# Performance work log

Hardware: AMD Instinct MI355X
Metric: run time of the kernel (lower is better)

## Reference

```python
import jax, jax.numpy as jnp
import numpy as np

B, N, DIM = 4, 2048, 512
HEADS, DIM_HEAD = 8, 64
INNER = HEADS * DIM_HEAD  # == DIM, so to_out is Identity
LN_EPS = 1e-5
MASK_FILL = 1e-8  # faithful to torch.where(mask, attn, 1e-08)


def setup_inputs() -> dict:
    key = jax.random.key(0)
    k1, k2 = jax.random.split(key)
    x = jax.random.normal(k1, (B, N, DIM), dtype=jnp.float32)
    gamma = jnp.ones((DIM,), dtype=jnp.float32)
    beta = jnp.zeros((DIM,), dtype=jnp.float32)
    w_qkv = jax.random.normal(k2, (3 * INNER, DIM), dtype=jnp.float32) * (DIM ** -0.5)
    mask = jnp.tril(jnp.ones((N, N), dtype=bool))  # causal boolean mask, asserted 2-D in source
    return {"x": x, "gamma": gamma, "beta": beta, "w_qkv": w_qkv, "mask": mask}


def reference(x, gamma, beta, w_qkv, mask):
    # LayerNorm over last dim
    mu = jnp.mean(x, axis=-1, keepdims=True)
    var = jnp.var(x, axis=-1, keepdims=True)
    h = (x - mu) * jax.lax.rsqrt(var + LN_EPS) * gamma + beta
    # qkv projection (no bias), chunk into q, k, v
    qkv = h @ w_qkv.T  # [B, N, 3*INNER]
    q, k, v = jnp.split(qkv, 3, axis=-1)

    def to_heads(t):  # b n (h d) -> b h n d
        return t.reshape(B, N, HEADS, DIM_HEAD).transpose(0, 2, 1, 3)

    q, k, v = to_heads(q), to_heads(k), to_heads(v)
    # NOTE: original forward does NOT apply self.scale
    attn = jnp.einsum('bhnd,bhmd->bhnm', q, k)
    attn = jnp.where(mask[None, None, :, :], attn, MASK_FILL)
    p = jax.nn.softmax(attn, axis=-1)
    out = jnp.einsum('bhnm,bhmd->bhnd', p, v)
    out = out.transpose(0, 2, 1, 3).reshape(B, N, INNER)  # b h n d -> b n (h d)
    return out  # to_out is Identity since INNER == DIM
```

## Files before the change

### kernel.cpp

```cpp
#include <hip/hip_runtime.h>
#include <hip/hip_bf16.h>
#include <math.h>

#define B_  4
#define N_  2048
#define DIM_ 512
#define HEADS_ 8
#define QKV_ 1536
#define MASK_C 1e-8f
#define M_FIX 12.0f
#define LOG2E 1.44269504f

typedef __bf16 bf16_t;
typedef bf16_t bf16x8 __attribute__((ext_vector_type(8)));
typedef float  f32x4  __attribute__((ext_vector_type(4)));

__device__ __forceinline__ bf16_t f2b(float x) { return (bf16_t)x; }
__device__ __forceinline__ float  b2f(bf16_t x) { return (float)x; }

__device__ __forceinline__ f32x4 mfma16(bf16x8 a, bf16x8 b, f32x4 c) {
    return __builtin_amdgcn_mfma_f32_16x16x32_bf16(a, b, c, 0, 0, 0);
}

__global__ __launch_bounds__(256) void ln_wsplit_kernel(const float* __restrict__ x,
                                                        const float* __restrict__ gamma,
                                                        const float* __restrict__ beta,
                                                        bf16_t* __restrict__ hh,
                                                        bf16_t* __restrict__ hl,
                                                        const float* __restrict__ wq,
                                                        bf16_t* __restrict__ wh,
                                                        bf16_t* __restrict__ wl) {
    int blk = blockIdx.x;
    int t = threadIdx.x;
    if (blk >= B_ * N_) {
        int i = ((blk - B_ * N_) * 256 + t) * 4;
        float4 v = *(const float4*)&wq[i];
        float vv[4] = {v.x, v.y, v.z, v.w};
        #pragma unroll
        for (int j = 0; j < 4; j++) {
            bf16_t hi = f2b(vv[j]);
            wh[i + j] = hi;
            wl[i + j] = f2b(vv[j] - b2f(hi));
        }
        return;
    }
    int row = blk;
    const float* xr = x + (size_t)row * DIM_;
    float2 xv = *(const float2*)&xr[2 * t];
    float e0 = xv.x, e1 = xv.y;
    float s  = e0 + e1;
    float sq = e0 * e0 + e1 * e1;
    for (int off = 32; off; off >>= 1) {
        s  += __shfl_xor(s, off);
        sq += __shfl_xor(sq, off);
    }
    __shared__ float red[8];
    int w = t >> 6;
    if ((t & 63) == 0) { red[w] = s; red[4 + w] = sq; }
    __syncthreads();
    float S  = red[0] + red[1] + red[2] + red[3];
    float SQ = red[4] + red[5] + red[6] + red[7];
    float mu = S * (1.0f / DIM_);
    float var = SQ * (1.0f / DIM_) - mu * mu;
    float rs = rsqrtf(var + 1e-5f);
    float2 gv = *(const float2*)&gamma[2 * t];
    float2 bv = *(const float2*)&beta[2 * t];
    float y0 = (e0 - mu) * rs * gv.x + bv.x;
    float y1 = (e1 - mu) * rs * gv.y + bv.y;
    size_t base = (size_t)row * DIM_ + 2 * t;
    bf16_t h0 = f2b(y0), h1 = f2b(y1);
    __align__(4) bf16_t hp[2] = {h0, h1};
    __align__(4) bf16_t lp[2] = {f2b(y0 - b2f(h0)), f2b(y1 - b2f(h1))};
    *(unsigned int*)&hh[base] = *(unsigned int*)hp;
    *(unsigned int*)&hl[base] = *(unsigned int*)lp;
}

__global__ __launch_bounds__(256, 3) void qkv_gemm(const bf16_t* __restrict__ hh,
                                                   const bf16_t* __restrict__ hl,
                                                   const bf16_t* __restrict__ wh,
                                                   const bf16_t* __restrict__ wl,
                                                   bf16_t* __restrict__ qh, bf16_t* __restrict__ ql,
                                                   bf16_t* __restrict__ kh, bf16_t* __restrict__ kl,
                                                   bf16_t* __restrict__ vth,
                                                   float* __restrict__ part) {
    __shared__ __align__(16) bf16_t smem[20480];
    bf16_t* Ah = smem;
    bf16_t* Al = smem + 5120;
    bf16_t* Bh = smem + 10240;
    bf16_t* Bl = smem + 15360;
    int bm = blockIdx.x & 63;
    int bn = blockIdx.x >> 6;
    int t = threadIdx.x;
    int w = t >> 6, lane = t & 63, quad = lane >> 4, l16 = lane & 15;

    f32x4 acc[2][8];
    #pragma unroll
    for (int i = 0; i < 2; i++)
        #pragma unroll
        for (int j = 0; j < 8; j++) acc[i][j] = (f32x4)(0.0f);

    int sr = t >> 1, skc = (t & 1) * 16;
    size_t gA = (size_t)(bm * 128 + sr) * 512 + skc;
    size_t gB = (size_t)(bn * 128 + sr) * 512 + skc;

    uint4 rAh0 = *(const uint4*)&hh[gA];
    uint4 rAh1 = *(const uint4*)&hh[gA + 8];
    uint4 rAl0 = *(const uint4*)&hl[gA];
    uint4 rAl1 = *(const uint4*)&hl[gA + 8];
    uint4 rBh0 = *(const uint4*)&wh[gB];
    uint4 rBh1 = *(const uint4*)&wh[gB + 8];
    uint4 rBl0 = *(const uint4*)&wl[gB];
    uint4 rBl1 = *(const uint4*)&wl[gB + 8];

    for (int k0 = 0; k0 < 512; k0 += 32) {
        __syncthreads();
        *(uint4*)&Ah[sr * 40 + skc]     = rAh0;
        *(uint4*)&Ah[sr * 40 + skc + 8] = rAh1;
        *(uint4*)&Al[sr * 40 + skc]     = rAl0;
        *(uint4*)&Al[sr * 40 + skc + 8] = rAl1;
        *(uint4*)&Bh[sr * 40 + skc]     = rBh0;
        *(uint4*)&Bh[sr * 40 + skc + 8] = rBh1;
        *(uint4*)&Bl[sr * 40 + skc]     = rBl0;
        *(uint4*)&Bl[sr * 40 + skc + 8] = rBl1;
        __syncthreads();

        if (k0 < 480) {
            int kn = k0 + 32;
            rAh0 = *(const uint4*)&hh[gA + kn];
            rAh1 = *(const uint4*)&hh[gA + kn + 8];
            rAl0 = *(const uint4*)&hl[gA + kn];
            rAl1 = *(const uint4*)&hl[gA + kn + 8];
            rBh0 = *(const uint4*)&wh[gB + kn];
            rBh1 = *(const uint4*)&wh[gB + kn + 8];
            rBl0 = *(const uint4*)&wl[gB + kn];
            rBl1 = *(const uint4*)&wl[gB + kn + 8];
        }

        bf16x8 aH[2], aL[2];
        #pragma unroll
        for (int mt = 0; mt < 2; mt++) {
            aH[mt] = *(const bf16x8*)&Ah[(w * 32 + mt * 16 + l16) * 40 + quad * 8];
            aL[mt] = *(const bf16x8*)&Al[(w * 32 + mt * 16 + l16) * 40 + quad * 8];
        }
        #pragma unroll
        for (int nt = 0; nt < 8; nt++) {
            bf16x8 bH = *(const bf16x8*)&Bh[(nt * 16 + l16) * 40 + quad * 8];
            bf16x8 bL = *(const bf16x8*)&Bl[(nt * 16 + l16) * 40 + quad * 8];
            #pragma unroll
            for (int mt = 0; mt < 2; mt++) {
                acc[mt][nt] = mfma16(aH[mt], bH, acc[mt][nt]);
                acc[mt][nt] = mfma16(aH[mt], bL, acc[mt][nt]);
                acc[mt][nt] = mfma16(aL[mt], bH, acc[mt][nt]);
            }
        }
    }

    if (bn < 8) {
        #pragma unroll
        for (int mt = 0; mt < 2; mt++)
            #pragma unroll
            for (int nt = 0; nt < 8; nt++)
                #pragma unroll
                for (int reg = 0; reg < 4; reg++) {
                    float v = acc[mt][nt][reg];
                    int row = bm * 128 + w * 32 + mt * 16 + quad * 4 + reg;
                    int n = bn * 128 + nt * 16 + l16;
                    bf16_t hi = f2b(v);
                    bf16_t lo = f2b(v - b2f(hi));
                    if (n < 512) {
                        size_t a = (size_t)row * 512 + n;
                        qh[a] = hi; ql[a] = lo;
                    } else {
                        size_t a = (size_t)row * 512 + (n - 512);
                        kh[a] = hi; kl[a] = lo;
                    }
                }
    } else {
        int bb = bm >> 4, key0 = (bm & 15) * 128;
        int n = t & 127, mc = (t >> 7) * 64;
        int head = (bn - 8) * 2 + (n >> 6), dd = n & 63;
        size_t obase = ((size_t)((bb * 8 + head) * 64 + dd)) * 2048 + key0 + mc;
        float Ssum = 0.0f;
        #pragma unroll
        for (int pass = 0; pass < 2; pass++) {
            __syncthreads();
            #pragma unroll
            for (int mt = 0; mt < 2; mt++)
                #pragma unroll
                for (int nt = 0; nt < 8; nt++)
                    #pragma unroll
                    for (int reg = 0; reg < 4; reg++) {
                        float v = acc[mt][nt][reg];
                        bf16_t hi = f2b(v);
                        bf16_t val = pass ? f2b(v - b2f(hi)) : hi;
                        smem[(w * 32 + mt * 16 + quad * 4 + reg) * 132 + nt * 16 + l16] = val;
                    }
            __syncthreads();
            #pragma unroll
            for (int i = 0; i < 64; i += 8) {
                __align__(16) bf16_t v8[8];
                #pragma unroll
                for (int j = 0; j < 8; j++) {
                    v8[j] = smem[(mc + i + j) * 132 + n];
                    Ssum += b2f(v8[j]);
                }
                if (pass == 0)
                    *(uint4*)&vth[obase + i] = *(const uint4*)v8;
            }
        }
        int tt = (key0 >> 6) + (mc >> 6);
        part[((size_t)((bb * 8 + head) * 32 + tt)) * 64 + dd] = Ssum;
    }
}

__global__ __launch_bounds__(256, 4) void attn_kernel(const bf16_t* __restrict__ qh,
                                                      const bf16_t* __restrict__ ql,
                                                      const bf16_t* __restrict__ kh,
                                                      const bf16_t* __restrict__ kl,
                                                      const bf16_t* __restrict__ vth,
                                                      const float* __restrict__ part,
                                                      float* __restrict__ out) {
    __shared__ __align__(16) bf16_t smem[17152];
    __shared__ float sufl[4][64];
    char* lds = (char*)smem;
    bf16_t* Ps = smem + 12288;

    int blk = blockIdx.x;
    int bh = blk & 31;
    int gi = blk >> 5;
    int g3 = gi & 7;
    int q4 = gi >> 3;
    int rt;
    if (q4 == 0)      rt = 31 - g3;
    else if (q4 == 1) rt = g3;
    else if (q4 == 2) rt = 23 - g3;
    else              rt = 8 + g3;
    int b = bh >> 3, head = bh & 7;
    int t = threadIdx.x;
    int w = t >> 6, lane = t & 63, quad = lane >> 4, l16 = lane & 15;

    {
        int d = t & 63, g = t >> 6;
        float s = 0.0f;
        for (int tt = rt + 1 + g; tt < 32; tt += 4)
            s += part[((size_t)bh * 32 + tt) * 64 + d];
        sufl[g][d] = s;
    }

    bf16x8 qAH[2], qAL[2];
    {
        int qrow = rt * 64 + w * 16 + l16;
        size_t g = ((size_t)(b * N_ + qrow)) * 512 + head * 64 + quad * 8;
        qAH[0] = *(const bf16x8*)&qh[g];
        qAH[1] = *(const bf16x8*)&qh[g + 32];
        qAL[0] = *(const bf16x8*)&ql[g];
        qAL[1] = *(const bf16x8*)&ql[g + 32];
    }
    bf16x8 ones;
    #pragma unroll
    for (int j = 0; j < 8; j++) ones[j] = f2b(1.0f);

    f32x4 O[4];
    #pragma unroll
    for (int nt = 0; nt < 4; nt++) O[nt] = (f32x4)(0.0f);
    f32x4 Lacc = (f32x4)(0.0f);
    const float mbias = M_FIX * LOG2E;

    int r = t >> 2, c16 = t & 3;
    int swz = (r & 7) << 4;
    int lk0 = r * 128 + ((c16 * 32)      ^ swz);
    int lk1 = r * 128 + ((c16 * 32 + 16) ^ swz);
    size_t gk = ((size_t)(b * N_ + r)) * 512 + head * 64 + c16 * 16;
    size_t gv = ((size_t)(bh * 64 + r)) * 2048 + c16 * 16;

    uint4 pKh0 = *(const uint4*)&kh[gk];
    uint4 pKh1 = *(const uint4*)&kh[gk + 8];
    uint4 pKl0 = *(const uint4*)&kl[gk];
    uint4 pKl1 = *(const uint4*)&kl[gk + 8];
    uint4 pVh0 = *(const uint4*)&vth[gv];
    uint4 pVh1 = *(const uint4*)&vth[gv + 8];

    for (int jt = 0; jt <= rt; jt++) {
        __syncthreads();
        *(uint4*)(lds + lk0)         = pKh0;
        *(uint4*)(lds + lk1)         = pKh1;
        *(uint4*)(lds + 8192 + lk0)  = pKl0;
        *(uint4*)(lds + 8192 + lk1)  = pKl1;
        *(uint4*)(lds + 16384 + lk0) = pVh0;
        *(uint4*)(lds + 16384 + lk1) = pVh1;
        __syncthreads();

        if (jt < rt) {
            gk += (size_t)64 * 512;
            gv += 64;
            pKh0 = *(const uint4*)&kh[gk];
            pKh1 = *(const uint4*)&kh[gk + 8];
            pKl0 = *(const uint4*)&kl[gk];
            pKl1 = *(const uint4*)&kl[gk + 8];
            pVh0 = *(const uint4*)&vth[gv];
            pVh1 = *(const uint4*)&vth[gv + 8];
        }

        f32x4 S[4];
        #pragma unroll
        for (int nt = 0; nt < 4; nt++) S[nt] = (f32x4)(0.0f);
        __builtin_amdgcn_s_setprio(1);
        #pragma unroll
        for (int khf = 0; khf < 2; khf++) {
            #pragma unroll
            for (int nt = 0; nt < 4; nt++) {
                int row = nt * 16 + l16;
                int bc = (khf * 64 + quad * 16) ^ ((row & 7) << 4);
                bf16x8 bH = *(const bf16x8*)(lds + row * 128 + bc);
                bf16x8 bL = *(const bf16x8*)(lds + 8192 + row * 128 + bc);
                S[nt] = mfma16(qAH[khf], bH, S[nt]);
                S[nt] = mfma16(qAH[khf], bL, S[nt]);
                S[nt] = mfma16(qAL[khf], bH, S[nt]);
            }
        }
        __builtin_amdgcn_s_setprio(0);

        if (jt == rt) {
            int lrow = w * 16 + quad * 4;
            #pragma unroll
            for (int nt = 0; nt < 4; nt++)
                #pragma unroll
                for (int reg = 0; reg < 4; reg++)
                    if (nt * 16 + l16 > lrow + reg) S[nt][reg] = MASK_C;
        }

        #pragma unroll
        for (int nt = 0; nt < 4; nt++)
            #pragma unroll
            for (int reg = 0; reg < 4; reg++)
                Ps[(w * 16 + quad * 4 + reg) * 76 + nt * 16 + l16] =
                    f2b(exp2f(fmaf(S[nt][reg], LOG2E, -mbias)));

        bf16x8 pH[2];
        #pragma unroll
        for (int khf = 0; khf < 2; khf++)
            pH[khf] = *(const bf16x8*)&Ps[(w * 16 + l16) * 76 + khf * 32 + quad * 8];

        __builtin_amdgcn_s_setprio(1);
        #pragma unroll
        for (int khf = 0; khf < 2; khf++) Lacc = mfma16(pH[khf], ones, Lacc);

        #pragma unroll
        for (int khf = 0; khf < 2; khf++) {
            #pragma unroll
            for (int nt = 0; nt < 4; nt++) {
                int row = nt * 16 + l16;
                int bc = (khf * 64 + quad * 16) ^ ((row & 7) << 4);
                bf16x8 vB = *(const bf16x8*)(lds + 16384 + row * 128 + bc);
                O[nt] = mfma16(pH[khf], vB, O[nt]);
            }
        }
        __builtin_amdgcn_s_setprio(0);
    }

    float L[4];
    #pragma unroll
    for (int reg = 0; reg < 4; reg++) L[reg] = Lacc[reg];
    int cnt = N_ - (rt + 1) * 64;
    if (cnt > 0) {
        float pc = expf(MASK_C - M_FIX);
        float sv[4];
        #pragma unroll
        for (int nt = 0; nt < 4; nt++) {
            int d = nt * 16 + l16;
            sv[nt] = sufl[0][d] + sufl[1][d] + sufl[2][d] + sufl[3][d];
        }
        #pragma unroll
        for (int reg = 0; reg < 4; reg++) {
            L[reg] += pc * (float)cnt;
            #pragma unroll
            for (int nt = 0; nt < 4; nt++) O[nt][reg] += pc * sv[nt];
        }
    }

    #pragma unroll
    for (int reg = 0; reg < 4; reg++) {
        float rl = 1.0f / L[reg];
        int row = rt * 64 + w * 16 + quad * 4 + reg;
        #pragma unroll
        for (int nt = 0; nt < 4; nt++)
            out[((size_t)(b * N_ + row)) * DIM_ + head * 64 + nt * 16 + l16] =
                O[nt][reg] * rl;
    }
}

extern "C" void kernel_launch(void* const* d_in, const int* in_sizes, int n_in,
                              void* d_out, int out_size, void* d_ws, size_t ws_size,
                              hipStream_t stream) {
    const float* x     = (const float*)d_in[0];
    const float* gamma = (const float*)d_in[1];
    const float* beta  = (const float*)d_in[2];
    const float* w_qkv = (const float*)d_in[3];
    float* out = (float*)d_out;

    const size_t HW = (size_t)8192 * 512;
    const size_t WN = (size_t)1536 * 512;
    bf16_t* hh  = (bf16_t*)d_ws;
    bf16_t* hl  = hh + HW;
    bf16_t* qh  = hl + HW;
    bf16_t* ql  = qh + HW;
    bf16_t* kh  = ql + HW;
    bf16_t* kl  = kh + HW;
    bf16_t* vth = kl + HW;
    bf16_t* vtl = vth + HW;
    bf16_t* wh  = vtl + HW;
    bf16_t* wl  = wh + WN;
    float*  part = (float*)(wl + WN);

    ln_wsplit_kernel<<<B_ * N_ + 768, 256, 0, stream>>>(x, gamma, beta, hh, hl,
                                                        w_qkv, wh, wl);
    qkv_gemm<<<768, 256, 0, stream>>>(hh, hl, wh, wl, qh, ql, kh, kl, vth, part);
    attn_kernel<<<1024, 256, 0, stream>>>(qh, ql, kh, kl, vth, part, out);
}
```

Baseline: 193.3 us.

## Split long causal attention rows into two KV-range blocks with a combine kernel

Query tiles 16-31 are each split into two blocks covering disjoint KV ranges, assigned through lookup tables for load balance. The grid grows from 1024 to 1536 blocks, and the split blocks write partial O (as bf16 hi/lo pairs) and partial L to workspace. A new fin kernel sums the two partials and normalizes. The three split-precision MFMA chains now go into separate accumulators to break the dependency chain. The cost is an extra launch plus partial-output traffic through global memory.

```diff
diff --git a/kernel.cpp b/kernel.cpp
--- a/kernel.cpp
+++ b/kernel.cpp
@@ -21,6 +21,19 @@
 __device__ __forceinline__ f32x4 mfma16(bf16x8 a, bf16x8 b, f32x4 c) {
     return __builtin_amdgcn_mfma_f32_16x16x32_bf16(a, b, c, 0, 0, 0);
 }
+
+__device__ const unsigned char TRT[48] = {
+    15,31,31,30,29,29,28,14,  30,28,27,27,26,13,12,24,
+    26,25,25,24,23,23,22,11,  20,19, 9,22,21,21,20,10,
+    19,18,18,17,17,16, 8,16,   0, 1, 2, 3, 4, 5, 6, 7};
+__device__ const unsigned char TJ0[48] = {
+     0, 0,16,15, 0,15,14, 0,   0, 0, 0,14,13, 0, 0,12,
+     0, 0,13, 0, 0,12,11, 0,   0,10, 0, 0, 0,11,10, 0,
+     0, 9, 0, 0, 9, 8, 0, 0,   0, 0, 0, 0, 0, 0, 0, 0};
+__device__ const unsigned char TJ1[48] = {
+    15,15,31,30,14,29,28,14,  14,13,13,27,26,13,12,24,
+    12,12,25,11,11,23,22,11,   9,19, 9,10,10,21,20,10,
+     9,18, 8, 8,17,16, 8, 7,   0, 1, 2, 3, 4, 5, 6, 7};
 
 __global__ __launch_bounds__(256) void ln_wsplit_kernel(const float* __restrict__ x,
                                                         const float* __restrict__ gamma,
@@ -219,6 +232,9 @@
                                                       const bf16_t* __restrict__ kl,
                                                       const bf16_t* __restrict__ vth,
                                                       const float* __restrict__ part,
+                                                      bf16_t* __restrict__ POh,
+                                                      bf16_t* __restrict__ POl,
+                                                      float* __restrict__ Lp,
                                                       float* __restrict__ out) {
     __shared__ __align__(16) bf16_t smem[17152];
     __shared__ float sufl[4][64];
@@ -228,18 +244,15 @@
     int blk = blockIdx.x;
     int bh = blk & 31;
     int gi = blk >> 5;
-    int g3 = gi & 7;
-    int q4 = gi >> 3;
-    int rt;
-    if (q4 == 0)      rt = 31 - g3;
-    else if (q4 == 1) rt = g3;
-    else if (q4 == 2) rt = 23 - g3;
-    else              rt = 8 + g3;
+    int rt = TRT[gi];
+    int j0 = TJ0[gi];
+    int j1 = TJ1[gi];
+    int isfin = (j1 == rt);
     int b = bh >> 3, head = bh & 7;
     int t = threadIdx.x;
     int w = t >> 6, lane = t & 63, quad = lane >> 4, l16 = lane & 15;
 
-    {
+    if (isfin) {
         int d = t & 63, g = t >> 6;
         float s = 0.0f;
         for (int tt = rt + 1 + g; tt < 32; tt += 4)
@@ -270,8 +283,8 @@
     int swz = (r & 7) << 4;
     int lk0 = r * 128 + ((c16 * 32)      ^ swz);
     int lk1 = r * 128 + ((c16 * 32 + 16) ^ swz);
-    size_t gk = ((size_t)(b * N_ + r)) * 512 + head * 64 + c16 * 16;
-    size_t gv = ((size_t)(bh * 64 + r)) * 2048 + c16 * 16;
+    size_t gk = ((size_t)(b * N_ + j0 * 64 + r)) * 512 + head * 64 + c16 * 16;
+    size_t gv = ((size_t)(bh * 64 + r)) * 2048 + j0 * 64 + c16 * 16;
 
     uint4 pKh0 = *(const uint4*)&kh[gk];
     uint4 pKh1 = *(const uint4*)&kh[gk + 8];
@@ -280,7 +293,7 @@
     uint4 pVh0 = *(const uint4*)&vth[gv];
     uint4 pVh1 = *(const uint4*)&vth[gv + 8];
 
-    for (int jt = 0; jt <= rt; jt++) {
+    for (int jt = j0; jt <= j1; jt++) {
         __syncthreads();
         *(uint4*)(lds + lk0)         = pKh0;
         *(uint4*)(lds + lk1)         = pKh1;
@@ -290,7 +303,7 @@
         *(uint4*)(lds + 16384 + lk1) = pVh1;
         __syncthreads();
 
-        if (jt < rt) {
+        if (jt < j1) {
             gk += (size_t)64 * 512;
             gv += 64;
             pKh0 = *(const uint4*)&kh[gk];
@@ -301,9 +314,11 @@
             pVh1 = *(const uint4*)&vth[gv + 8];
         }
 
-        f32x4 S[4];
-        #pragma unroll
-        for (int nt = 0; nt < 4; nt++) S[nt] = (f32x4)(0.0f);
+        f32x4 S1[4], S2[4], S3[4];
+        #pragma unroll
+        for (int nt = 0; nt < 4; nt++) {
+            S1[nt] = (f32x4)(0.0f); S2[nt] = (f32x4)(0.0f); S3[nt] = (f32x4)(0.0f);
+        }
         __builtin_amdgcn_s_setprio(1);
         #pragma unroll
         for (int khf = 0; khf < 2; khf++) {
@@ -313,12 +328,14 @@
                 int bc = (khf * 64 + quad * 16) ^ ((row & 7) << 4);
                 bf16x8 bH = *(const bf16x8*)(lds + row * 128 + bc);
                 bf16x8 bL = *(const bf16x8*)(lds + 8192 + row * 128 + bc);
-                S[nt] = mfma16(qAH[khf], bH, S[nt]);
-                S[nt] = mfma16(qAH[khf], bL, S[nt]);
-                S[nt] = mfma16(qAL[khf], bH, S[nt]);
+                S1[nt] = mfma16(qAH[khf], bH, S1[nt]);
+                S2[nt] = mfma16(qAH[khf], bL, S2[nt]);
+                S3[nt] = mfma16(qAL[khf], bH, S3[nt]);
             }
         }
         __builtin_amdgcn_s_setprio(0);
+        #pragma unroll
+        for (int nt = 0; nt < 4; nt++) S1[nt] = S1[nt] + S2[nt] + S3[nt];
 
         if (jt == rt) {
             int lrow = w * 16 + quad * 4;
@@ -326,7 +343,7 @@
             for (int nt = 0; nt < 4; nt++)
                 #pragma unroll
                 for (int reg = 0; reg < 4; reg++)
-                    if (nt * 16 + l16 > lrow + reg) S[nt][reg] = MASK_C;
+                    if (nt * 16 + l16 > lrow + reg) S1[nt][reg] = MASK_C;
         }
 
         #pragma unroll
@@ -334,7 +351,7 @@
             #pragma unroll
             for (int reg = 0; reg < 4; reg++)
                 Ps[(w * 16 + quad * 4 + reg) * 76 + nt * 16 + l16] =
-                    f2b(exp2f(fmaf(S[nt][reg], LOG2E, -mbias)));
+                    f2b(exp2f(fmaf(S1[nt][reg], LOG2E, -mbias)));
 
         bf16x8 pH[2];
         #pragma unroll
@@ -361,8 +378,9 @@
     float L[4];
     #pragma unroll
     for (int reg = 0; reg < 4; reg++) L[reg] = Lacc[reg];
+
     int cnt = N_ - (rt + 1) * 64;
-    if (cnt > 0) {
+    if (isfin && cnt > 0) {
         float pc = expf(MASK_C - M_FIX);
         float sv[4];
         #pragma unroll
@@ -378,14 +396,60 @@
         }
     }
 
+    if (rt < 16) {
+        #pragma unroll
+        for (int reg = 0; reg < 4; reg++) {
+            float rl = 1.0f / L[reg];
+            int row = rt * 64 + w * 16 + quad * 4 + reg;
+            #pragma unroll
+            for (int nt = 0; nt < 4; nt++)
+                out[((size_t)(b * N_ + row)) * DIM_ + head * 64 + nt * 16 + l16] =
+                    O[nt][reg] * rl;
+        }
+    } else {
+        int pidx = ((bh << 4) + (rt - 16)) * 2 + isfin;
+        #pragma unroll
+        for (int reg = 0; reg < 4; reg++) {
+            int lrow = w * 16 + quad * 4 + reg;
+            size_t base = ((size_t)pidx * 64 + lrow) * 64;
+            #pragma unroll
+            for (int nt = 0; nt < 4; nt++) {
+                float v = O[nt][reg];
+                bf16_t hi = f2b(v);
+                POh[base + nt * 16 + l16] = hi;
+                POl[base + nt * 16 + l16] = f2b(v - b2f(hi));
+            }
+            if (l16 == 0) Lp[pidx * 64 + lrow] = L[reg];
+        }
+    }
+}
+
+__global__ __launch_bounds__(256) void fin_kernel(const bf16_t* __restrict__ POh,
+                                                  const bf16_t* __restrict__ POl,
+                                                  const float* __restrict__ Lp,
+                                                  float* __restrict__ out) {
+    int blk = blockIdx.x;
+    int bh = blk & 31, rt = 16 + (blk >> 5);
+    int b = bh >> 3, head = bh & 7;
+    int t = threadIdx.x;
+    int r = t >> 2, dq = t & 3;
+    int p0 = ((bh << 4) + (rt - 16)) * 2, p1 = p0 + 1;
+    float rl = 1.0f / (Lp[p0 * 64 + r] + Lp[p1 * 64 + r]);
+    size_t b0 = ((size_t)p0 * 64 + r) * 64 + dq * 16;
+    size_t b1 = ((size_t)p1 * 64 + r) * 64 + dq * 16;
+    size_t ob = ((size_t)(b * N_ + rt * 64 + r)) * 512 + head * 64 + dq * 16;
     #pragma unroll
-    for (int reg = 0; reg < 4; reg++) {
-        float rl = 1.0f / L[reg];
-        int row = rt * 64 + w * 16 + quad * 4 + reg;
-        #pragma unroll
-        for (int nt = 0; nt < 4; nt++)
-            out[((size_t)(b * N_ + row)) * DIM_ + head * 64 + nt * 16 + l16] =
-                O[nt][reg] * rl;
+    for (int g = 0; g < 2; g++) {
+        bf16x8 ah = *(const bf16x8*)&POh[b0 + g * 8];
+        bf16x8 al = *(const bf16x8*)&POl[b0 + g * 8];
+        bf16x8 ch = *(const bf16x8*)&POh[b1 + g * 8];
+        bf16x8 cl = *(const bf16x8*)&POl[b1 + g * 8];
+        float res[8];
+        #pragma unroll
+        for (int j = 0; j < 8; j++)
+            res[j] = (b2f(ah[j]) + b2f(al[j]) + b2f(ch[j]) + b2f(cl[j])) * rl;
+        *(float4*)&out[ob + g * 8]     = make_float4(res[0], res[1], res[2], res[3]);
+        *(float4*)&out[ob + g * 8 + 4] = make_float4(res[4], res[5], res[6], res[7]);
     }
 }
 
@@ -407,13 +471,17 @@
     bf16_t* kh  = ql + HW;
     bf16_t* kl  = kh + HW;
     bf16_t* vth = kl + HW;
-    bf16_t* vtl = vth + HW;
-    bf16_t* wh  = vtl + HW;
+    bf16_t* POh = vth + HW;
+    bf16_t* wh  = POh + HW;
     bf16_t* wl  = wh + WN;
     float*  part = (float*)(wl + WN);
+    bf16_t* POl = (bf16_t*)(part + (size_t)32 * 32 * 64);
+    float*  Lp  = (float*)(POl + HW);
 
     ln_wsplit_kernel<<<B_ * N_ + 768, 256, 0, stream>>>(x, gamma, beta, hh, hl,
                                                         w_qkv, wh, wl);
     qkv_gemm<<<768, 256, 0, stream>>>(hh, hl, wh, wl, qh, ql, kh, kl, vth, part);
-    attn_kernel<<<1024, 256, 0, stream>>>(qh, ql, kh, kl, vth, part, out);
-}
+    attn_kernel<<<1536, 256, 0, stream>>>(qh, ql, kh, kl, vth, part,
+                                          POh, POl, Lp, out);
+    fin_kernel<<<512, 256, 0, stream>>>(POh, POl, Lp, out);
+}
```

Result: slower. 230.0 us (+19.0%).
